# Kernel tuning notes

Hardware: AMD Instinct MI355X
Metric: run time of the kernel (lower is better)

## Reference

```python
import jax, jax.numpy as jnp
import numpy as np

H = 1024   # hidden_size
I = 2048   # intermediate_size
E = 16     # num_experts
K = 2      # num_experts_per_tok
B, T = 2, 2048


def setup_inputs() -> dict:
    key = jax.random.key(0)
    k1, k2, k3, k4 = jax.random.split(key, 4)
    x = jax.random.normal(k1, (B, T, H), dtype=jnp.float32)
    # torch nn.Linear weight layout: [out_features, in_features]
    Wg = jax.random.normal(k2, (E, H), dtype=jnp.float32) * 0.02   # gate
    W1 = jax.random.normal(k3, (E, I, H), dtype=jnp.float32) * 0.02  # fc1 per expert
    W2 = jax.random.normal(k4, (E, H, I), dtype=jnp.float32) * 0.02  # fc2 per expert
    return {"x": x, "Wg": Wg, "W1": W1, "W2": W2}


def reference(x, Wg, W1, W2):
    Bq, Tq, Hq = x.shape
    nt = Bq * Tq
    x_flat = x.reshape(nt, Hq)                       # [nt, H]
    gate_logits = x_flat @ Wg.T                      # [nt, E]
    gate_probs = jax.nn.softmax(gate_logits, axis=-1)
    topk_vals, topk_idx = jax.lax.top_k(gate_probs, K)  # [nt, K]
    # dense combine weights: zero for unselected (token, expert) pairs
    rows = jnp.arange(nt)[:, None]                   # [nt, 1]
    cw = jnp.zeros((nt, E), dtype=x.dtype).at[rows, topk_idx].add(topk_vals)
    # per-expert dense SiLU-MLP; combine weight of 0 makes unselected
    # contributions exactly zero, matching the original gather/scatter math.
    y_flat = jnp.zeros_like(x_flat)
    for e in range(E):
        h = jax.nn.silu(x_flat @ W1[e].T)            # [nt, I]
        o = h @ W2[e].T                              # [nt, H]
        y_flat = y_flat + cw[:, e:e + 1] * o
    return y_flat.reshape(Bq, Tq, Hq)
```

## Files before the change

kernel.cpp:

```cpp
#include <hip/hip_runtime.h>
#include <hip/hip_bf16.h>

#define H_DIM 1024
#define I_DIM 2048
#define NEXP  16
#define NTOK  4096
#define BM 128
#define BN 128
#define BK 32
#define MAXS 10240
#define MAXRB (MAXS/BM)
#define PAIRS (NTOK*2)
#define SORT_T 256
#define PPT (PAIRS/SORT_T)

typedef __attribute__((ext_vector_type(8))) short short8;
typedef __attribute__((ext_vector_type(4))) short short4v;
typedef __attribute__((ext_vector_type(4))) float f32x4;

#define OFF_TOKE 256
#define OFF_TOKW (OFF_TOKE + PAIRS*4)
#define OFF_TOS  (OFF_TOKW + PAIRS*4)
#define OFF_WOS  (OFF_TOS + MAXS*4)
#define OFF_H    (OFF_WOS + MAXS*4)
#define OFF_XBF  (OFF_H + (size_t)MAXS*I_DIM*2)
#define OFF_WBF  (OFF_XBF + (size_t)NTOK*H_DIM*2)
#define NEED_FULL (OFF_WBF + (size_t)NEXP*I_DIM*H_DIM*2)

#define GLDS16(gsrc, ldst) \
  __builtin_amdgcn_global_load_lds((const __attribute__((address_space(1))) void*)(gsrc), \
                                   (__attribute__((address_space(3))) void*)(ldst), 16, 0, 0)

__device__ inline short f2bf(float f) {
    union { float f; unsigned u; } v; v.f = f;
    unsigned u = v.u + 0x7FFFu + ((v.u >> 16) & 1u);
    return (short)(u >> 16);
}

__device__ inline short8 pack8(const float4 a, const float4 b) {
    return (short8){ f2bf(a.x), f2bf(a.y), f2bf(a.z), f2bf(a.w),
                     f2bf(b.x), f2bf(b.y), f2bf(b.z), f2bf(b.w) };
}

__global__ __launch_bounds__(256) void conv_kernel(
    const float* __restrict__ src, short* __restrict__ dst, int n8)
{
    int i = blockIdx.x * blockDim.x + threadIdx.x;
    const int stride = gridDim.x * blockDim.x;
    for (; i < n8; i += stride) {
        const float4 f0 = ((const float4*)src)[2*i];
        const float4 f1 = ((const float4*)src)[2*i+1];
        ((short8*)dst)[i] = pack8(f0, f1);
    }
}

template<bool WRITE_XBF>
__global__ __launch_bounds__(256) void gate_kernel(
    const float* __restrict__ x, const float* __restrict__ Wg,
    int* __restrict__ tokE, float* __restrict__ tokW, short* __restrict__ xbf)
{
    const int tok  = blockIdx.x * 4 + (threadIdx.x >> 6);
    const int lane = threadIdx.x & 63;
    const float4* xr = (const float4*)(x + (size_t)tok * H_DIM);

    float acc[NEXP];
#pragma unroll
    for (int e = 0; e < NEXP; e++) acc[e] = 0.f;
#pragma unroll
    for (int j = 0; j < H_DIM/4; j += 64) {
        const float4 xv = xr[j + lane];
        if constexpr (WRITE_XBF) {
            *(short4v*)(xbf + (size_t)tok * H_DIM + (j + lane) * 4) =
                (short4v){ f2bf(xv.x), f2bf(xv.y), f2bf(xv.z), f2bf(xv.w) };
        }
#pragma unroll
        for (int e = 0; e < NEXP; e++) {
            const float4 wv = ((const float4*)(Wg + e * H_DIM))[j + lane];
            acc[e] = fmaf(xv.x, wv.x, fmaf(xv.y, wv.y, fmaf(xv.z, wv.z, fmaf(xv.w, wv.w, acc[e]))));
        }
    }
#pragma unroll
    for (int off = 32; off; off >>= 1) {
#pragma unroll
        for (int e = 0; e < NEXP; e++) acc[e] += __shfl_xor(acc[e], off, 64);
    }
    if (lane == 0) {
        float m = acc[0];
#pragma unroll
        for (int e = 1; e < NEXP; e++) m = fmaxf(m, acc[e]);
        float p[NEXP]; float s = 0.f;
#pragma unroll
        for (int e = 0; e < NEXP; e++) { p[e] = __expf(acc[e] - m); s += p[e]; }
        int i1 = 0;
#pragma unroll
        for (int e = 1; e < NEXP; e++) if (acc[e] > acc[i1]) i1 = e;
        int i2 = -1;
#pragma unroll
        for (int e = 0; e < NEXP; e++) {
            if (e == i1) continue;
            if (i2 < 0 || acc[e] > acc[i2]) i2 = e;
        }
        const float inv = 1.f / s;
        tokE[tok*2+0] = i1; tokW[tok*2+0] = p[i1] * inv;
        tokE[tok*2+1] = i2; tokW[tok*2+1] = p[i2] * inv;
    }
}

__global__ __launch_bounds__(SORT_T) void sort_kernel(
    const int* __restrict__ tokE, const float* __restrict__ tokW,
    int* __restrict__ aoff, int* __restrict__ tok_of_slot, float* __restrict__ w_of_slot)
{
    __shared__ int hist[NEXP * SORT_T];
    __shared__ int tot[NEXP];
    __shared__ int aoff_l[NEXP + 1];

    const int tid = threadIdx.x;
    const int lane = tid & 63, wv = tid >> 6;

    int eloc[PPT];
#pragma unroll
    for (int i = 0; i < PPT; i++) eloc[i] = tokE[tid * PPT + i];

#pragma unroll
    for (int e = 0; e < NEXP; e++) hist[e * SORT_T + tid] = 0;
    __syncthreads();
#pragma unroll
    for (int i = 0; i < PPT; i++) hist[eloc[i] * SORT_T + tid]++;
    __syncthreads();

#pragma unroll
    for (int r = 0; r < 4; r++) {
        const int e = wv * 4 + r;
        const int base = e * SORT_T + lane * 4;
        int v0 = hist[base+0], v1 = hist[base+1], v2 = hist[base+2], v3 = hist[base+3];
        const int s = v0 + v1 + v2 + v3;
        int incl = s;
#pragma unroll
        for (int off = 1; off < 64; off <<= 1) {
            const int t = __shfl_up(incl, off, 64);
            if (lane >= off) incl += t;
        }
        int run = incl - s;
        hist[base+0] = run; run += v0;
        hist[base+1] = run; run += v1;
        hist[base+2] = run; run += v2;
        hist[base+3] = run;
        if (lane == 63) tot[e] = incl;
    }
    __syncthreads();

    if (tid == 0) {
        int acc = 0;
#pragma unroll
        for (int e = 0; e < NEXP; e++) {
            aoff_l[e] = acc; aoff[e] = acc;
            acc += ((tot[e] + BM - 1) / BM) * BM;
        }
        aoff_l[NEXP] = acc; aoff[NEXP] = acc;
    }
    __syncthreads();

#pragma unroll
    for (int i = 0; i < PPT; i++) {
        const int p = tid * PPT + i;
        const int e = eloc[i];
        const int idx = hist[e * SORT_T + tid]++;
        const int slot = aoff_l[e] + idx;
        tok_of_slot[slot] = p >> 1;
        w_of_slot[slot] = tokW[p];
    }
}

template<int MODE>
__global__ __launch_bounds__(256) void fc1_kernel_t(
    const void* __restrict__ xsrc, const void* __restrict__ w1src,
    const int* __restrict__ aoff, const int* __restrict__ tok_of_slot,
    short* __restrict__ h)
{
    const int total = aoff[NEXP];
    const int row0 = blockIdx.y * BM;
    if (row0 >= total) return;
    int e = 0;
    while (aoff[e+1] <= row0) e++;
    const int col0 = blockIdx.x * BN;

    __shared__ short As[BM*BK];
    __shared__ short Bs[BN*BK];

    const int tid = threadIdx.x, wid = tid>>6, lane = tid&63;
    const int wr = wid>>1, wc = wid&1;

    const int srow = wid*32 + (lane>>2);
    const int skc  = (lane&3)*8;

    int t0 = tok_of_slot[row0 + srow];      if (t0 < 0) t0 = 0;
    int t1 = tok_of_slot[row0 + srow + 16]; if (t1 < 0) t1 = 0;

    const short *sa0=nullptr,*sa1=nullptr,*sb0=nullptr,*sb1=nullptr;
    const float *fa0=nullptr,*fa1=nullptr,*fb0=nullptr,*fb1=nullptr;
    if constexpr (MODE == 0) {
        const short* xb = (const short*)xsrc;
        const short* wb = (const short*)w1src + (size_t)e * I_DIM * H_DIM;
        sa0 = xb + (size_t)t0 * H_DIM + skc;
        sa1 = xb + (size_t)t1 * H_DIM + skc;
        sb0 = wb + (size_t)(col0 + srow)      * H_DIM + skc;
        sb1 = wb + (size_t)(col0 + srow + 16) * H_DIM + skc;
    } else {
        const float* xf = (const float*)xsrc;
        const float* wf = (const float*)w1src + (size_t)e * I_DIM * H_DIM;
        fa0 = xf + (size_t)t0 * H_DIM + skc;
        fa1 = xf + (size_t)t1 * H_DIM + skc;
        fb0 = wf + (size_t)(col0 + srow)      * H_DIM + skc;
        fb1 = wf + (size_t)(col0 + srow + 16) * H_DIM + skc;
    }
    short* la0 = &As[(wid*2+0)*512];
    short* la1 = &As[(wid*2+1)*512];
    short* lb0 = &Bs[(wid*2+0)*512];
    short* lb1 = &Bs[(wid*2+1)*512];

    const int frow = lane & 15, fko = (lane>>4)*8;

    f32x4 acc[4][4];
#pragma unroll
    for (int m=0;m<4;m++)
#pragma unroll
        for (int n=0;n<4;n++) acc[m][n] = (f32x4){0.f,0.f,0.f,0.f};

    for (int k0 = 0; k0 < H_DIM; k0 += BK) {
        if constexpr (MODE == 0) {
            GLDS16(sa0 + k0, la0);
            GLDS16(sa1 + k0, la1);
            GLDS16(sb0 + k0, lb0);
            GLDS16(sb1 + k0, lb1);
        } else {
            const float4 a00 = *(const float4*)(fa0 + k0), a01 = *(const float4*)(fa0 + k0 + 4);
            const float4 a10 = *(const float4*)(fa1 + k0), a11 = *(const float4*)(fa1 + k0 + 4);
            const float4 b00 = *(const float4*)(fb0 + k0), b01 = *(const float4*)(fb0 + k0 + 4);
            const float4 b10 = *(const float4*)(fb1 + k0), b11 = *(const float4*)(fb1 + k0 + 4);
            *(short8*)&As[srow*32 + skc]      = pack8(a00, a01);
            *(short8*)&As[(srow+16)*32 + skc] = pack8(a10, a11);
            *(short8*)&Bs[srow*32 + skc]      = pack8(b00, b01);
            *(short8*)&Bs[(srow+16)*32 + skc] = pack8(b10, b11);
        }
        __syncthreads();

        short8 af[4], bfr[4];
#pragma unroll
        for (int m=0;m<4;m++) af[m]  = *(const short8*)&As[(wr*64 + m*16 + frow)*32 + fko];
#pragma unroll
        for (int n=0;n<4;n++) bfr[n] = *(const short8*)&Bs[(wc*64 + n*16 + frow)*32 + fko];
#pragma unroll
        for (int m=0;m<4;m++)
#pragma unroll
            for (int n=0;n<4;n++)
                acc[m][n] = __builtin_amdgcn_mfma_f32_16x16x32_bf16(af[m], bfr[n], acc[m][n], 0, 0, 0);
        __syncthreads();
    }

    const int mr0 = row0 + wr*64 + (lane>>4)*4;
    const int nc0 = col0 + wc*64 + (lane&15);
#pragma unroll
    for (int m=0;m<4;m++)
#pragma unroll
        for (int n=0;n<4;n++)
#pragma unroll
            for (int r=0;r<4;r++) {
                const float v = acc[m][n][r];
                const float sv = v / (1.f + __expf(-v));
                h[(size_t)(mr0 + m*16 + r) * I_DIM + nc0 + n*16] = f2bf(sv);
            }
}

template<int MODE, int KS>
__global__ __launch_bounds__(256) void fc2_kernel_t(
    const short* __restrict__ h, const void* __restrict__ w2src,
    const int* __restrict__ aoff, const int* __restrict__ tok_of_slot,
    const float* __restrict__ w_of_slot, float* __restrict__ y)
{
    const int total = aoff[NEXP];
    const int row0 = blockIdx.y * BM;
    if (row0 >= total) return;
    int e = 0;
    while (aoff[e+1] <= row0) e++;
    const int ks   = blockIdx.x % KS;
    const int col0 = (blockIdx.x / KS) * BN;
    const int kbeg = ks * (I_DIM / KS);
    const int kend = kbeg + (I_DIM / KS);

    __shared__ short As[BM*BK];
    __shared__ short Bs[BN*BK];

    const int tid = threadIdx.x, wid = tid>>6, lane = tid&63;
    const int wr = wid>>1, wc = wid&1;

    const int srow = wid*32 + (lane>>2);
    const int skc  = (lane&3)*8;

    const short* sa0 = h + (size_t)(row0 + srow)      * I_DIM + skc;
    const short* sa1 = h + (size_t)(row0 + srow + 16) * I_DIM + skc;

    const short *sb0=nullptr,*sb1=nullptr;
    const float *fb0=nullptr,*fb1=nullptr;
    if constexpr (MODE == 0) {
        const short* wb = (const short*)w2src + (size_t)e * H_DIM * I_DIM;
        sb0 = wb + (size_t)(col0 + srow)      * I_DIM + skc;
        sb1 = wb + (size_t)(col0 + srow + 16) * I_DIM + skc;
    } else {
        const float* wf = (const float*)w2src + (size_t)e * H_DIM * I_DIM;
        fb0 = wf + (size_t)(col0 + srow)      * I_DIM + skc;
        fb1 = wf + (size_t)(col0 + srow + 16) * I_DIM + skc;
    }
    short* la0 = &As[(wid*2+0)*512];
    short* la1 = &As[(wid*2+1)*512];
    short* lb0 = &Bs[(wid*2+0)*512];
    short* lb1 = &Bs[(wid*2+1)*512];

    const int frow = lane & 15, fko = (lane>>4)*8;

    f32x4 acc[4][4];
#pragma unroll
    for (int m=0;m<4;m++)
#pragma unroll
        for (int n=0;n<4;n++) acc[m][n] = (f32x4){0.f,0.f,0.f,0.f};

    for (int k0 = kbeg; k0 < kend; k0 += BK) {
        GLDS16(sa0 + k0, la0);
        GLDS16(sa1 + k0, la1);
        if constexpr (MODE == 0) {
            GLDS16(sb0 + k0, lb0);
            GLDS16(sb1 + k0, lb1);
        } else {
            const float4 b00 = *(const float4*)(fb0 + k0), b01 = *(const float4*)(fb0 + k0 + 4);
            const float4 b10 = *(const float4*)(fb1 + k0), b11 = *(const float4*)(fb1 + k0 + 4);
            *(short8*)&Bs[srow*32 + skc]      = pack8(b00, b01);
            *(short8*)&Bs[(srow+16)*32 + skc] = pack8(b10, b11);
        }
        __syncthreads();

        short8 af[4], bfr[4];
#pragma unroll
        for (int m=0;m<4;m++) af[m]  = *(const short8*)&As[(wr*64 + m*16 + frow)*32 + fko];
#pragma unroll
        for (int n=0;n<4;n++) bfr[n] = *(const short8*)&Bs[(wc*64 + n*16 + frow)*32 + fko];
#pragma unroll
        for (int m=0;m<4;m++)
#pragma unroll
            for (int n=0;n<4;n++)
                acc[m][n] = __builtin_amdgcn_mfma_f32_16x16x32_bf16(af[m], bfr[n], acc[m][n], 0, 0, 0);
        __syncthreads();
    }

    const int mr0 = row0 + wr*64 + (lane>>4)*4;
    const int nc0 = col0 + wc*64 + (lane&15);
#pragma unroll
    for (int m=0;m<4;m++)
#pragma unroll
        for (int r=0;r<4;r++) {
            const int slot = mr0 + m*16 + r;
            const int tok = tok_of_slot[slot];
            if (tok < 0) continue;
            const float w = w_of_slot[slot];
#pragma unroll
            for (int n=0;n<4;n++)
                atomicAdd(&y[(size_t)tok * H_DIM + nc0 + n*16], w * acc[m][n][r]);
        }
}

extern "C" void kernel_launch(void* const* d_in, const int* in_sizes, int n_in,
                              void* d_out, int out_size, void* d_ws, size_t ws_size,
                              hipStream_t stream) {
    const float* x  = (const float*)d_in[0];
    const float* Wg = (const float*)d_in[1];
    const float* W1 = (const float*)d_in[2];
    const float* W2 = (const float*)d_in[3];
    float* y = (float*)d_out;

    char* ws = (char*)d_ws;
    int*   aoff        = (int*)  (ws + 128);
    int*   tokE        = (int*)  (ws + OFF_TOKE);
    float* tokW        = (float*)(ws + OFF_TOKW);
    int*   tok_of_slot = (int*)  (ws + OFF_TOS);
    float* w_of_slot   = (float*)(ws + OFF_WOS);
    short* h           = (short*)(ws + OFF_H);
    short* xbf         = (short*)(ws + OFF_XBF);
    short* wbf         = (short*)(ws + OFF_WBF);

    const bool full = (ws_size >= NEED_FULL);

    hipMemsetAsync(tok_of_slot, 0xFF, MAXS*4, stream);
    hipMemsetAsync(y, 0, (size_t)out_size * 4, stream);

    if (full) {
        gate_kernel<true><<<NTOK/4, 256, 0, stream>>>(x, Wg, tokE, tokW, xbf);
        sort_kernel<<<1, SORT_T, 0, stream>>>(tokE, tokW, aoff, tok_of_slot, w_of_slot);
        conv_kernel<<<2048, 256, 0, stream>>>(W1, wbf, NEXP*I_DIM*H_DIM/8);
        fc1_kernel_t<0><<<dim3(I_DIM/BN, MAXRB), 256, 0, stream>>>(xbf, wbf, aoff, tok_of_slot, h);
        conv_kernel<<<2048, 256, 0, stream>>>(W2, wbf, NEXP*H_DIM*I_DIM/8);
        fc2_kernel_t<0,2><<<dim3((H_DIM/BN)*2, MAXRB), 256, 0, stream>>>(h, wbf, aoff, tok_of_slot, w_of_slot, y);
    } else {
        gate_kernel<false><<<NTOK/4, 256, 0, stream>>>(x, Wg, tokE, tokW, nullptr);
        sort_kernel<<<1, SORT_T, 0, stream>>>(tokE, tokW, aoff, tok_of_slot, w_of_slot);
        fc1_kernel_t<1><<<dim3(I_DIM/BN, MAXRB), 256, 0, stream>>>(x, W1, aoff, tok_of_slot, h);
        fc2_kernel_t<1,1><<<dim3(H_DIM/BN, MAXRB), 256, 0, stream>>>(h, W2, aoff, tok_of_slot, w_of_slot, y);
    }
}
```

Baseline: 283.7 us.

## Double-buffer LDS tiles in fc1/fc2 and drop fc2 split-K

Both expert GEMM kernels now use two shared-memory buffers, so the next K-tile is loaded while MFMAs run on the current tile, and one barrier per iteration is removed. The fc2 kernel also drops its two-way split-K, so each block covers the full intermediate dimension and issues half as many atomic adds. This doubles LDS use per block, which may lower occupancy, and halves the fc2 grid, which reduces parallelism.

```diff
diff --git a/kernel.cpp b/kernel.cpp
--- a/kernel.cpp
+++ b/kernel.cpp
@@ -8,6 +8,8 @@
 #define BM 128
 #define BN 128
 #define BK 32
+#define ABUF (BM*BK)
+#define BBUF (BN*BK)
 #define MAXS 10240
 #define MAXRB (MAXS/BM)
 #define PAIRS (NTOK*2)
@@ -184,8 +186,8 @@
     while (aoff[e+1] <= row0) e++;
     const int col0 = blockIdx.x * BN;
 
-    __shared__ short As[BM*BK];
-    __shared__ short Bs[BN*BK];
+    __shared__ short As[2*ABUF];
+    __shared__ short Bs[2*BBUF];
 
     const int tid = threadIdx.x, wid = tid>>6, lane = tid&63;
     const int wr = wid>>1, wc = wid&1;
@@ -226,36 +228,46 @@
 #pragma unroll
         for (int n=0;n<4;n++) acc[m][n] = (f32x4){0.f,0.f,0.f,0.f};
 
-    for (int k0 = 0; k0 < H_DIM; k0 += BK) {
-        if constexpr (MODE == 0) {
-            GLDS16(sa0 + k0, la0);
-            GLDS16(sa1 + k0, la1);
-            GLDS16(sb0 + k0, lb0);
-            GLDS16(sb1 + k0, lb1);
-        } else {
-            const float4 a00 = *(const float4*)(fa0 + k0), a01 = *(const float4*)(fa0 + k0 + 4);
-            const float4 a10 = *(const float4*)(fa1 + k0), a11 = *(const float4*)(fa1 + k0 + 4);
-            const float4 b00 = *(const float4*)(fb0 + k0), b01 = *(const float4*)(fb0 + k0 + 4);
-            const float4 b10 = *(const float4*)(fb1 + k0), b11 = *(const float4*)(fb1 + k0 + 4);
-            *(short8*)&As[srow*32 + skc]      = pack8(a00, a01);
-            *(short8*)&As[(srow+16)*32 + skc] = pack8(a10, a11);
-            *(short8*)&Bs[srow*32 + skc]      = pack8(b00, b01);
-            *(short8*)&Bs[(srow+16)*32 + skc] = pack8(b10, b11);
-        }
-        __syncthreads();
+#define FC1_STAGE(buf, k)                                                     \
+    if constexpr (MODE == 0) {                                                \
+        GLDS16(sa0 + (k), la0 + (buf)*ABUF);                                  \
+        GLDS16(sa1 + (k), la1 + (buf)*ABUF);                                  \
+        GLDS16(sb0 + (k), lb0 + (buf)*BBUF);                                  \
+        GLDS16(sb1 + (k), lb1 + (buf)*BBUF);                                  \
+    } else {                                                                  \
+        const float4 a00 = *(const float4*)(fa0+(k)), a01 = *(const float4*)(fa0+(k)+4); \
+        const float4 a10 = *(const float4*)(fa1+(k)), a11 = *(const float4*)(fa1+(k)+4); \
+        const float4 b00 = *(const float4*)(fb0+(k)), b01 = *(const float4*)(fb0+(k)+4); \
+        const float4 b10 = *(const float4*)(fb1+(k)), b11 = *(const float4*)(fb1+(k)+4); \
+        *(short8*)&As[(buf)*ABUF + srow*32 + skc]      = pack8(a00, a01);     \
+        *(short8*)&As[(buf)*ABUF + (srow+16)*32 + skc] = pack8(a10, a11);     \
+        *(short8*)&Bs[(buf)*BBUF + srow*32 + skc]      = pack8(b00, b01);     \
+        *(short8*)&Bs[(buf)*BBUF + (srow+16)*32 + skc] = pack8(b10, b11);     \
+    }
+
+    FC1_STAGE(0, 0);
+    __syncthreads();
+
+    const int NT = H_DIM / BK;
+    int cur = 0;
+    for (int t = 0; t < NT; ++t) {
+        if (t + 1 < NT) { FC1_STAGE(cur ^ 1, (t + 1) * BK); }
 
         short8 af[4], bfr[4];
 #pragma unroll
-        for (int m=0;m<4;m++) af[m]  = *(const short8*)&As[(wr*64 + m*16 + frow)*32 + fko];
-#pragma unroll
-        for (int n=0;n<4;n++) bfr[n] = *(const short8*)&Bs[(wc*64 + n*16 + frow)*32 + fko];
+        for (int m=0;m<4;m++) af[m]  = *(const short8*)&As[cur*ABUF + (wr*64 + m*16 + frow)*32 + fko];
+#pragma unroll
+        for (int n=0;n<4;n++) bfr[n] = *(const short8*)&Bs[cur*BBUF + (wc*64 + n*16 + frow)*32 + fko];
 #pragma unroll
         for (int m=0;m<4;m++)
 #pragma unroll
             for (int n=0;n<4;n++)
                 acc[m][n] = __builtin_amdgcn_mfma_f32_16x16x32_bf16(af[m], bfr[n], acc[m][n], 0, 0, 0);
+
         __syncthreads();
-    }
+        cur ^= 1;
+    }
+#undef FC1_STAGE
 
     const int mr0 = row0 + wr*64 + (lane>>4)*4;
     const int nc0 = col0 + wc*64 + (lane&15);
@@ -271,7 +283,7 @@
             }
 }
 
-template<int MODE, int KS>
+template<int MODE>
 __global__ __launch_bounds__(256) void fc2_kernel_t(
     const short* __restrict__ h, const void* __restrict__ w2src,
     const int* __restrict__ aoff, const int* __restrict__ tok_of_slot,
@@ -282,13 +294,10 @@
     if (row0 >= total) return;
     int e = 0;
     while (aoff[e+1] <= row0) e++;
-    const int ks   = blockIdx.x % KS;
-    const int col0 = (blockIdx.x / KS) * BN;
-    const int kbeg = ks * (I_DIM / KS);
-    const int kend = kbeg + (I_DIM / KS);
-
-    __shared__ short As[BM*BK];
-    __shared__ short Bs[BN*BK];
+    const int col0 = blockIdx.x * BN;
+
+    __shared__ short As[2*ABUF];
+    __shared__ short Bs[2*BBUF];
 
     const int tid = threadIdx.x, wid = tid>>6, lane = tid&63;
     const int wr = wid>>1, wc = wid&1;
@@ -323,32 +332,44 @@
 #pragma unroll
         for (int n=0;n<4;n++) acc[m][n] = (f32x4){0.f,0.f,0.f,0.f};
 
-    for (int k0 = kbeg; k0 < kend; k0 += BK) {
-        GLDS16(sa0 + k0, la0);
-        GLDS16(sa1 + k0, la1);
-        if constexpr (MODE == 0) {
-            GLDS16(sb0 + k0, lb0);
-            GLDS16(sb1 + k0, lb1);
-        } else {
-            const float4 b00 = *(const float4*)(fb0 + k0), b01 = *(const float4*)(fb0 + k0 + 4);
-            const float4 b10 = *(const float4*)(fb1 + k0), b11 = *(const float4*)(fb1 + k0 + 4);
-            *(short8*)&Bs[srow*32 + skc]      = pack8(b00, b01);
-            *(short8*)&Bs[(srow+16)*32 + skc] = pack8(b10, b11);
-        }
-        __syncthreads();
+#define FC2_STAGE(buf, k)                                                     \
+    {                                                                         \
+        GLDS16(sa0 + (k), la0 + (buf)*ABUF);                                  \
+        GLDS16(sa1 + (k), la1 + (buf)*ABUF);                                  \
+        if constexpr (MODE == 0) {                                            \
+            GLDS16(sb0 + (k), lb0 + (buf)*BBUF);                              \
+            GLDS16(sb1 + (k), lb1 + (buf)*BBUF);                              \
+        } else {                                                              \
+            const float4 b00 = *(const float4*)(fb0+(k)), b01 = *(const float4*)(fb0+(k)+4); \
+            const float4 b10 = *(const float4*)(fb1+(k)), b11 = *(const float4*)(fb1+(k)+4); \
+            *(short8*)&Bs[(buf)*BBUF + srow*32 + skc]      = pack8(b00, b01); \
+            *(short8*)&Bs[(buf)*BBUF + (srow+16)*32 + skc] = pack8(b10, b11); \
+        }                                                                     \
+    }
+
+    FC2_STAGE(0, 0);
+    __syncthreads();
+
+    const int NT = I_DIM / BK;
+    int cur = 0;
+    for (int t = 0; t < NT; ++t) {
+        if (t + 1 < NT) { FC2_STAGE(cur ^ 1, (t + 1) * BK); }
 
         short8 af[4], bfr[4];
 #pragma unroll
-        for (int m=0;m<4;m++) af[m]  = *(const short8*)&As[(wr*64 + m*16 + frow)*32 + fko];
-#pragma unroll
-        for (int n=0;n<4;n++) bfr[n] = *(const short8*)&Bs[(wc*64 + n*16 + frow)*32 + fko];
+        for (int m=0;m<4;m++) af[m]  = *(const short8*)&As[cur*ABUF + (wr*64 + m*16 + frow)*32 + fko];
+#pragma unroll
+        for (int n=0;n<4;n++) bfr[n] = *(const short8*)&Bs[cur*BBUF + (wc*64 + n*16 + frow)*32 + fko];
 #pragma unroll
         for (int m=0;m<4;m++)
 #pragma unroll
             for (int n=0;n<4;n++)
                 acc[m][n] = __builtin_amdgcn_mfma_f32_16x16x32_bf16(af[m], bfr[n], acc[m][n], 0, 0, 0);
+
         __syncthreads();
-    }
+        cur ^= 1;
+    }
+#undef FC2_STAGE
 
     const int mr0 = row0 + wr*64 + (lane>>4)*4;
     const int nc0 = col0 + wc*64 + (lane&15);
@@ -396,11 +417,11 @@
         conv_kernel<<<2048, 256, 0, stream>>>(W1, wbf, NEXP*I_DIM*H_DIM/8);
         fc1_kernel_t<0><<<dim3(I_DIM/BN, MAXRB), 256, 0, stream>>>(xbf, wbf, aoff, tok_of_slot, h);
         conv_kernel<<<2048, 256, 0, stream>>>(W2, wbf, NEXP*H_DIM*I_DIM/8);
-        fc2_kernel_t<0,2><<<dim3((H_DIM/BN)*2, MAXRB), 256, 0, stream>>>(h, wbf, aoff, tok_of_slot, w_of_slot, y);
+        fc2_kernel_t<0><<<dim3(H_DIM/BN, MAXRB), 256, 0, stream>>>(h, wbf, aoff, tok_of_slot, w_of_slot, y);
     } else {
         gate_kernel<false><<<NTOK/4, 256, 0, stream>>>(x, Wg, tokE, tokW, nullptr);
         sort_kernel<<<1, SORT_T, 0, stream>>>(tokE, tokW, aoff, tok_of_slot, w_of_slot);
         fc1_kernel_t<1><<<dim3(I_DIM/BN, MAXRB), 256, 0, stream>>>(x, W1, aoff, tok_of_slot, h);
-        fc2_kernel_t<1,1><<<dim3(H_DIM/BN, MAXRB), 256, 0, stream>>>(h, W2, aoff, tok_of_slot, w_of_slot, y);
-    }
-}
+        fc2_kernel_t<1><<<dim3(H_DIM/BN, MAXRB), 256, 0, stream>>>(h, W2, aoff, tok_of_slot, w_of_slot, y);
+    }
+}
```

Result: faster. 278.0 us (-2.0%).
